# Kernel tuning notes

Hardware: AMD Instinct MI355X
Metric: run time of the kernel (lower is better)

## Reference

```python
import jax, jax.numpy as jnp
import numpy as np

EPS = 1e-12  # torch F.normalize eps

def _l2norm(x, axis):
    n = jnp.linalg.norm(x, axis=axis, keepdims=True)
    return x / jnp.maximum(n, EPS)

def setup_inputs() -> dict:
    key = jax.random.key(0)
    ks = jax.random.split(key, 4)
    B, T, C, E, I = 2, 2048, 1024, 8, 2048
    return {
        "hidden_states": jax.random.normal(ks[0], (B, T, C), dtype=jnp.float32),
        "sim_matrix": jax.random.normal(ks[1], (C, E), dtype=jnp.float32),
        "gates": jnp.zeros((E,), dtype=jnp.float32),
        "temperature": jnp.float32(1.0),
        "experts_mask": jnp.ones((E,), dtype=jnp.float32),
        "w1": jax.random.normal(ks[2], (E, C, I), dtype=jnp.float32) * (1.0 / np.sqrt(C)),
        "w2": jax.random.normal(ks[3], (E, I, C), dtype=jnp.float32) * (1.0 / np.sqrt(I)),
        "min_experts": 2,
    }

def _gating(flat_h, sim_matrix, gates, temperature, experts_mask, min_experts):
    # flat_h: [N, C]
    logit_scale = jax.nn.sigmoid(temperature)
    logits = _l2norm(flat_h, -1) @ _l2norm(sim_matrix, 0)  # [N, E]
    logits = logits * experts_mask
    gated = jax.nn.relu(logits - gates * logit_scale)
    # GateSTE: forward hard threshold, backward identity
    act = gated + jax.lax.stop_gradient((gated > 0).astype(gated.dtype) - gated)
    # fallback: tokens with no active expert get top-min_experts by logits
    inactive = jnp.sum(act, axis=1) == 0  # [N]
    _, idx = jax.lax.top_k(logits, min_experts)  # [N, k]
    fallback = jnp.sum(jax.nn.one_hot(idx, logits.shape[1], dtype=act.dtype), axis=1) > 0  # [N, E] bool
    act = jnp.where(inactive[:, None] & fallback, jnp.asarray(1.0, act.dtype), act)
    return act, logits

def reference(hidden_states, sim_matrix, gates, temperature, experts_mask, w1, w2, min_experts):
    b, t, c = hidden_states.shape
    e = w1.shape[0]
    act, router_logits = _gating(hidden_states.reshape(b * t, c), sim_matrix, gates,
                                 temperature, experts_mask, min_experts)
    inter = jnp.einsum('btc,eci->btei', hidden_states, w1)
    inter = jax.nn.gelu(inter, approximate=False)
    expert_out = jnp.einsum('btei,eic->btec', inter, w2)
    mask = act.reshape(b, t, e)
    summed = jnp.sum(expert_out * mask[..., None], axis=-2)  # [b,t,c]
    num_act = jnp.clip(jnp.sum(mask, axis=-1, keepdims=True), 1, None)
    final = summed / num_act
    return final, router_logits, act
```

## Files before the change

kernel.cpp:

```cpp
#include <hip/hip_runtime.h>
#include <math.h>

typedef __bf16 bf16x8 __attribute__((ext_vector_type(8)));
typedef __bf16 bf16x4 __attribute__((ext_vector_type(4)));
typedef float  f32x4  __attribute__((ext_vector_type(4)));

#define NTOK 4096
#define CDIM 1024
#define EEXP 8
#define IDIM 2048

__device__ __forceinline__ void async_copy16(const __bf16* g, __bf16* l) {
  __builtin_amdgcn_global_load_lds((const __attribute__((address_space(1))) void*)g,
                                   (__attribute__((address_space(3))) void*)l,
                                   16, 0, 0);
}

__device__ __forceinline__ float gelu_f(float x) {
  float u = 0.7978845608028654f * fmaf(0.044715f * x * x, x, x);
  float ex = __expf(-2.f * fabsf(u));
  float th = copysignf((1.f - ex) / (1.f + ex), u);
  return 0.5f * x * (1.f + th);
}

__global__ __launch_bounds__(256) void gating_kernel(
    const float* __restrict__ h, const float* __restrict__ sim,
    const float* __restrict__ gates, const float* __restrict__ temp,
    const float* __restrict__ emask, const int* __restrict__ minexp,
    float* __restrict__ out_logits, float* __restrict__ out_act,
    float* __restrict__ inv_num, __bf16* __restrict__ hb)
{
  const int t = blockIdx.x, tid = threadIdx.x;
  float4 hv4 = ((const float4*)(h + (size_t)t * CDIM))[tid];
  float hv[4] = {hv4.x, hv4.y, hv4.z, hv4.w};
  bf16x4 hb4 = {(__bf16)hv[0], (__bf16)hv[1], (__bf16)hv[2], (__bf16)hv[3]};
  ((bf16x4*)(hb + (size_t)t * CDIM))[tid] = hb4;

  float d[EEXP], nn[EEXP];
  #pragma unroll
  for (int e = 0; e < EEXP; ++e) { d[e] = 0.f; nn[e] = 0.f; }
  float ss = 0.f;
  #pragma unroll
  for (int j = 0; j < 4; ++j) {
    ss = fmaf(hv[j], hv[j], ss);
    const float* sr = sim + (size_t)(tid * 4 + j) * EEXP;
    float4 s0 = ((const float4*)sr)[0];
    float4 s1 = ((const float4*)sr)[1];
    float sv[8] = {s0.x, s0.y, s0.z, s0.w, s1.x, s1.y, s1.z, s1.w};
    #pragma unroll
    for (int e = 0; e < EEXP; ++e) {
      d[e]  = fmaf(hv[j], sv[e], d[e]);
      nn[e] = fmaf(sv[e], sv[e], nn[e]);
    }
  }
  #pragma unroll
  for (int off = 32; off > 0; off >>= 1) {
    ss += __shfl_down(ss, off);
    #pragma unroll
    for (int e = 0; e < EEXP; ++e) {
      d[e]  += __shfl_down(d[e], off);
      nn[e] += __shfl_down(nn[e], off);
    }
  }
  __shared__ float red[4][20];
  const int wv = tid >> 6;
  if ((tid & 63) == 0) {
    red[wv][0] = ss;
    #pragma unroll
    for (int e = 0; e < EEXP; ++e) { red[wv][1 + e] = d[e]; red[wv][9 + e] = nn[e]; }
  }
  __syncthreads();
  if (tid == 0) {
    float sst = red[0][0] + red[1][0] + red[2][0] + red[3][0];
    float inv_h = 1.f / fmaxf(sqrtf(sst), 1e-12f);
    float ls = 1.f / (1.f + expf(-temp[0]));
    float logit[EEXP], act[EEXP];
    float cnt = 0.f;
    #pragma unroll
    for (int e = 0; e < EEXP; ++e) {
      float dot = red[0][1 + e] + red[1][1 + e] + red[2][1 + e] + red[3][1 + e];
      float nne = red[0][9 + e] + red[1][9 + e] + red[2][9 + e] + red[3][9 + e];
      float inv_s = 1.f / fmaxf(sqrtf(nne), 1e-12f);
      logit[e] = dot * inv_h * inv_s * emask[e];
      float g = logit[e] - gates[e] * ls;
      act[e] = (g > 0.f) ? 1.f : 0.f;
      cnt += act[e];
    }
    if (cnt == 0.f) {
      int k = minexp[0];
      if (k > EEXP) k = EEXP;
      bool used[EEXP];
      #pragma unroll
      for (int e = 0; e < EEXP; ++e) used[e] = false;
      for (int j = 0; j < k; ++j) {
        int best = -1; float bv = 0.f;
        for (int e = 0; e < EEXP; ++e)
          if (!used[e] && (best < 0 || logit[e] > bv)) { best = e; bv = logit[e]; }
        if (best >= 0) { used[best] = true; act[best] = 1.f; cnt += 1.f; }
      }
    }
    float num = fmaxf(cnt, 1.f);
    inv_num[t] = 1.f / num;
    #pragma unroll
    for (int e = 0; e < EEXP; ++e) {
      out_logits[(size_t)t * EEXP + e] = logit[e];
      out_act[(size_t)t * EEXP + e]   = act[e];
    }
  }
}

__global__ __launch_bounds__(64) void pack_kernel(
    const float* __restrict__ out_act, int* __restrict__ counts,
    unsigned short* __restrict__ perm)
{
  const int e = blockIdx.x;
  const int lane = threadIdx.x;
  const unsigned long long ltmask = (lane == 63) ? ~0ULL >> 1 : (1ULL << lane) - 1ULL;
  int base = 0;
  for (int i = 0; i < NTOK / 64; ++i) {
    int tok = i * 64 + lane;
    bool f = out_act[(size_t)tok * EEXP + e] > 0.f;
    unsigned long long m = __ballot(f);
    if (f) perm[e * NTOK + base + __popcll(m & ltmask)] = (unsigned short)tok;
    base += __popcll(m);
  }
  if (lane == 0) counts[e] = base;
}

__global__ __launch_bounds__(256) void transpose_f32_bf16(
    const float* __restrict__ in0, __bf16* __restrict__ out0, int R, int Cc,
    long sIn, long sOut)
{
  const float* in = in0 + (size_t)blockIdx.z * sIn;
  __bf16* out = out0 + (size_t)blockIdx.z * sOut;
  __shared__ __align__(16) __bf16 tile[64][72];
  const int tid = threadIdx.x;
  const int c0 = blockIdx.x * 64, r0 = blockIdx.y * 64;
  #pragma unroll
  for (int p = 0; p < 2; ++p) {
    int lin = p * 256 + tid;
    int r = lin >> 3, c8 = (lin & 7) * 8;
    const float* src = in + (size_t)(r0 + r) * Cc + c0 + c8;
    float4 v0 = ((const float4*)src)[0];
    float4 v1 = ((const float4*)src)[1];
    bf16x8 v = {(__bf16)v0.x, (__bf16)v0.y, (__bf16)v0.z, (__bf16)v0.w,
                (__bf16)v1.x, (__bf16)v1.y, (__bf16)v1.z, (__bf16)v1.w};
    *(bf16x8*)&tile[r][c8] = v;
  }
  __syncthreads();
  #pragma unroll
  for (int p = 0; p < 2; ++p) {
    int lin = p * 256 + tid;
    int oc = lin >> 3, j8 = (lin & 7) * 8;
    bf16x8 o;
    #pragma unroll
    for (int jj = 0; jj < 8; ++jj) o[jj] = tile[j8 + jj][oc];
    *(bf16x8*)(out + (size_t)(c0 + oc) * R + r0 + j8) = o;
  }
}

template <int MODE, int NN, int KK>
__global__ __launch_bounds__(256, 4) void gemm_pk(
    const __bf16* __restrict__ A0, const __bf16* __restrict__ B0,
    const int* __restrict__ counts, const unsigned short* __restrict__ perm,
    const float* __restrict__ inv_num, void* __restrict__ Cout)
{
  const int lin = blockIdx.x;
  const int e = lin & 7;
  const int q = lin >> 3;
  const int m0 = (q & 31) * 128;
  const int n0 = (q >> 5) * 128;
  const int Me = counts[e];
  if (m0 >= Me) return;
  const int tid = threadIdx.x;
  const int wave = tid >> 6, lane = tid & 63;
  const int wm = (wave >> 1) * 64, wn = (wave & 1) * 64;
  const int quad = lane >> 4, lrow = lane & 15;
  const int srow = lane >> 2;
  const int skol = (((lane & 3) ^ ((lane >> 3) & 3)) * 8);
  const int xk = (quad ^ ((lrow >> 1) & 3)) * 8;

  __shared__ __align__(16) __bf16 As[128 * 32];
  __shared__ __align__(16) __bf16 Bs[128 * 32];
  __bf16* lA = As + wave * 1024;
  __bf16* lB = Bs + wave * 1024;

  const unsigned short* pe = perm + e * NTOK;
  const int ra0 = m0 + wave * 32 + srow;
  const int ca0 = min(ra0, Me - 1), ca1 = min(ra0 + 16, Me - 1);
  const __bf16* Ab0;
  const __bf16* Ab1;
  if (MODE == 0) {
    Ab0 = A0 + (size_t)pe[ca0] * KK + skol;
    Ab1 = A0 + (size_t)pe[ca1] * KK + skol;
  } else {
    const __bf16* Abase = A0 + (size_t)e * NTOK * KK;
    Ab0 = Abase + (size_t)ca0 * KK + skol;
    Ab1 = Abase + (size_t)ca1 * KK + skol;
  }
  const __bf16* Bb = B0 + (size_t)e * (CDIM * IDIM)
                   + (size_t)(n0 + wave * 32 + srow) * KK + skol;

  f32x4 acc[4][4] = {};

  for (int k0 = 0; k0 < KK; k0 += 32) {
    async_copy16(Ab0 + k0, lA);
    async_copy16(Ab1 + k0, lA + 512);
    async_copy16(Bb + k0, lB);
    async_copy16(Bb + (size_t)16 * KK + k0, lB + 512);
    __syncthreads();
    bf16x8 af[4], bfr[4];
    #pragma unroll
    for (int mi = 0; mi < 4; ++mi)
      af[mi] = *(const bf16x8*)(As + (wm + mi * 16 + lrow) * 32 + xk);
    #pragma unroll
    for (int ni = 0; ni < 4; ++ni)
      bfr[ni] = *(const bf16x8*)(Bs + (wn + ni * 16 + lrow) * 32 + xk);
    #pragma unroll
    for (int mi = 0; mi < 4; ++mi)
      #pragma unroll
      for (int ni = 0; ni < 4; ++ni)
        acc[mi][ni] = __builtin_amdgcn_mfma_f32_16x16x32_bf16(af[mi], bfr[ni], acc[mi][ni], 0, 0, 0);
    __syncthreads();
  }

  if (MODE == 0) {
    __bf16* O = (__bf16*)Cout + (size_t)e * NTOK * NN;
    #pragma unroll
    for (int mi = 0; mi < 4; ++mi) {
      #pragma unroll
      for (int r = 0; r < 4; ++r) {
        const int row = m0 + wm + mi * 16 + quad * 4 + r;
        const float sv = inv_num[pe[min(row, Me - 1)]];
        #pragma unroll
        for (int ni = 0; ni < 4; ++ni) {
          const int col = n0 + wn + ni * 16 + lrow;
          O[(size_t)row * NN + col] = (__bf16)(gelu_f(acc[mi][ni][r]) * sv);
        }
      }
    }
  } else {
    float* O = (float*)Cout;
    #pragma unroll
    for (int mi = 0; mi < 4; ++mi) {
      #pragma unroll
      for (int r = 0; r < 4; ++r) {
        const int row = m0 + wm + mi * 16 + quad * 4 + r;
        if (row < Me) {
          const int tok = pe[row];
          #pragma unroll
          for (int ni = 0; ni < 4; ++ni) {
            const int col = n0 + wn + ni * 16 + lrow;
            atomicAdd(&O[(size_t)tok * NN + col], acc[mi][ni][r]);
          }
        }
      }
    }
  }
}

extern "C" void kernel_launch(void* const* d_in, const int* in_sizes, int n_in,
                              void* d_out, int out_size, void* d_ws, size_t ws_size,
                              hipStream_t stream) {
  (void)in_sizes; (void)n_in; (void)out_size; (void)ws_size;
  const float* h     = (const float*)d_in[0];
  const float* sim   = (const float*)d_in[1];
  const float* gates = (const float*)d_in[2];
  const float* temp  = (const float*)d_in[3];
  const float* emask = (const float*)d_in[4];
  const float* w1    = (const float*)d_in[5];
  const float* w2    = (const float*)d_in[6];
  const int*   minexp = (const int*)d_in[7];

  float* out_final  = (float*)d_out;
  float* out_logits = out_final + (size_t)NTOK * CDIM;
  float* out_act    = out_logits + (size_t)NTOK * EEXP;

  char* ws = (char*)d_ws;
  float*          inv_num  = (float*)(ws + 0);
  int*            counts   = (int*)(ws + 16384);
  unsigned short* perm     = (unsigned short*)(ws + 16448);
  __bf16*         hb       = (__bf16*)(ws + 81984);
  __bf16*         w1T_all  = (__bf16*)(ws + 8470592);
  __bf16*         w2T_all  = (__bf16*)(ws + 42025024);
  __bf16*         inter_pk = (__bf16*)(ws + 75579456);

  const long sW = (long)CDIM * IDIM;

  hipMemsetAsync(out_final, 0, (size_t)NTOK * CDIM * sizeof(float), stream);
  transpose_f32_bf16<<<dim3(IDIM / 64, CDIM / 64, EEXP), 256, 0, stream>>>(
      w1, w1T_all, CDIM, IDIM, sW, sW);
  transpose_f32_bf16<<<dim3(CDIM / 64, IDIM / 64, EEXP), 256, 0, stream>>>(
      w2, w2T_all, IDIM, CDIM, sW, sW);
  gating_kernel<<<NTOK, 256, 0, stream>>>(h, sim, gates, temp, emask, minexp,
                                          out_logits, out_act, inv_num, hb);
  pack_kernel<<<EEXP, 64, 0, stream>>>(out_act, counts, perm);
  gemm_pk<0, IDIM, CDIM><<<EEXP * (IDIM / 128) * (NTOK / 128), 256, 0, stream>>>(
      hb, w1T_all, counts, perm, inv_num, (void*)inter_pk);
  gemm_pk<1, CDIM, IDIM><<<EEXP * (CDIM / 128) * (NTOK / 128), 256, 0, stream>>>(
      inter_pk, w2T_all, counts, perm, inv_num, (void*)out_final);
}
```

Before: 477.2 us.

## Double-buffer LDS tiles to prefetch next K-slice during MFMA compute

```diff
diff --git a/kernel.cpp b/kernel.cpp
--- a/kernel.cpp
+++ b/kernel.cpp
@@ -180,10 +180,8 @@
   const int skol = (((lane & 3) ^ ((lane >> 3) & 3)) * 8);
   const int xk = (quad ^ ((lrow >> 1) & 3)) * 8;
 
-  __shared__ __align__(16) __bf16 As[128 * 32];
-  __shared__ __align__(16) __bf16 Bs[128 * 32];
-  __bf16* lA = As + wave * 1024;
-  __bf16* lB = Bs + wave * 1024;
+  __shared__ __align__(16) __bf16 As[2][128 * 32];
+  __shared__ __align__(16) __bf16 Bs[2][128 * 32];
 
   const unsigned short* pe = perm + e * NTOK;
   const int ra0 = m0 + wave * 32 + srow;
@@ -203,25 +201,37 @@
 
   f32x4 acc[4][4] = {};
 
-  for (int k0 = 0; k0 < KK; k0 += 32) {
-    async_copy16(Ab0 + k0, lA);
-    async_copy16(Ab1 + k0, lA + 512);
-    async_copy16(Bb + k0, lB);
-    async_copy16(Bb + (size_t)16 * KK + k0, lB + 512);
+  const int woff = wave * 1024;
+  async_copy16(Ab0, &As[0][woff]);
+  async_copy16(Ab1, &As[0][woff + 512]);
+  async_copy16(Bb, &Bs[0][woff]);
+  async_copy16(Bb + (size_t)16 * KK, &Bs[0][woff + 512]);
+
+  const int stages = KK / 32;
+  for (int s = 0; s < stages; ++s) {
     __syncthreads();
+    if (s + 1 < stages) {
+      const int k1 = (s + 1) * 32;
+      const int b1 = (s + 1) & 1;
+      async_copy16(Ab0 + k1, &As[b1][woff]);
+      async_copy16(Ab1 + k1, &As[b1][woff + 512]);
+      async_copy16(Bb + k1, &Bs[b1][woff]);
+      async_copy16(Bb + (size_t)16 * KK + k1, &Bs[b1][woff + 512]);
+    }
+    const __bf16* Asb = As[s & 1];
+    const __bf16* Bsb = Bs[s & 1];
     bf16x8 af[4], bfr[4];
     #pragma unroll
     for (int mi = 0; mi < 4; ++mi)
-      af[mi] = *(const bf16x8*)(As + (wm + mi * 16 + lrow) * 32 + xk);
+      af[mi] = *(const bf16x8*)(Asb + (wm + mi * 16 + lrow) * 32 + xk);
     #pragma unroll
     for (int ni = 0; ni < 4; ++ni)
-      bfr[ni] = *(const bf16x8*)(Bs + (wn + ni * 16 + lrow) * 32 + xk);
+      bfr[ni] = *(const bf16x8*)(Bsb + (wn + ni * 16 + lrow) * 32 + xk);
     #pragma unroll
     for (int mi = 0; mi < 4; ++mi)
       #pragma unroll
       for (int ni = 0; ni < 4; ++ni)
         acc[mi][ni] = __builtin_amdgcn_mfma_f32_16x16x32_bf16(af[mi], bfr[ni], acc[mi][ni], 0, 0, 0);
-    __syncthreads();
   }
 
   if (MODE == 0) {
```

Measured after the change: 484.4 us. About the same (+1.5%).

## Load GEMM fragments directly from global memory, bypassing LDS staging

Applied to the files above, without the earlier changes.

```diff
diff --git a/kernel.cpp b/kernel.cpp
--- a/kernel.cpp
+++ b/kernel.cpp
@@ -9,12 +9,6 @@
 #define CDIM 1024
 #define EEXP 8
 #define IDIM 2048
-
-__device__ __forceinline__ void async_copy16(const __bf16* g, __bf16* l) {
-  __builtin_amdgcn_global_load_lds((const __attribute__((address_space(1))) void*)g,
-                                   (__attribute__((address_space(3))) void*)l,
-                                   16, 0, 0);
-}
 
 __device__ __forceinline__ float gelu_f(float x) {
   float u = 0.7978845608028654f * fmaf(0.044715f * x * x, x, x);
@@ -127,19 +121,30 @@
   if (lane == 0) counts[e] = base;
 }
 
-__global__ __launch_bounds__(256) void transpose_f32_bf16(
-    const float* __restrict__ in0, __bf16* __restrict__ out0, int R, int Cc,
-    long sIn, long sOut)
-{
-  const float* in = in0 + (size_t)blockIdx.z * sIn;
-  __bf16* out = out0 + (size_t)blockIdx.z * sOut;
+__global__ __launch_bounds__(256) void transpose_all(
+    const float* __restrict__ w1, const float* __restrict__ w2,
+    __bf16* __restrict__ w1T, __bf16* __restrict__ w2T)
+{
+  const int lin = blockIdx.x;
+  const int slot = lin >> 9;
+  const int t = lin & 511;
+  const float* in; __bf16* out; int Cc, c0, r0;
+  if (slot < 8) {
+    in = w1 + (size_t)slot * CDIM * IDIM;
+    out = w1T + (size_t)slot * CDIM * IDIM;
+    Cc = IDIM; c0 = (t & 31) * 64; r0 = (t >> 5) * 64;
+  } else {
+    in = w2 + (size_t)(slot - 8) * CDIM * IDIM;
+    out = w2T + (size_t)(slot - 8) * CDIM * IDIM;
+    Cc = CDIM; c0 = (t & 15) * 64; r0 = (t >> 4) * 64;
+  }
+  const int R = (slot < 8) ? CDIM : IDIM;
   __shared__ __align__(16) __bf16 tile[64][72];
   const int tid = threadIdx.x;
-  const int c0 = blockIdx.x * 64, r0 = blockIdx.y * 64;
   #pragma unroll
   for (int p = 0; p < 2; ++p) {
-    int lin = p * 256 + tid;
-    int r = lin >> 3, c8 = (lin & 7) * 8;
+    int l2 = p * 256 + tid;
+    int r = l2 >> 3, c8 = (l2 & 7) * 8;
     const float* src = in + (size_t)(r0 + r) * Cc + c0 + c8;
     float4 v0 = ((const float4*)src)[0];
     float4 v1 = ((const float4*)src)[1];
@@ -150,8 +155,8 @@
   __syncthreads();
   #pragma unroll
   for (int p = 0; p < 2; ++p) {
-    int lin = p * 256 + tid;
-    int oc = lin >> 3, j8 = (lin & 7) * 8;
+    int l2 = p * 256 + tid;
+    int oc = l2 >> 3, j8 = (l2 & 7) * 8;
     bf16x8 o;
     #pragma unroll
     for (int jj = 0; jj < 8; ++jj) o[jj] = tile[j8 + jj][oc];
@@ -160,7 +165,7 @@
 }
 
 template <int MODE, int NN, int KK>
-__global__ __launch_bounds__(256, 4) void gemm_pk(
+__global__ __launch_bounds__(256) void gemm_rd(
     const __bf16* __restrict__ A0, const __bf16* __restrict__ B0,
     const int* __restrict__ counts, const unsigned short* __restrict__ perm,
     const float* __restrict__ inv_num, void* __restrict__ Cout)
@@ -176,52 +181,37 @@
   const int wave = tid >> 6, lane = tid & 63;
   const int wm = (wave >> 1) * 64, wn = (wave & 1) * 64;
   const int quad = lane >> 4, lrow = lane & 15;
-  const int srow = lane >> 2;
-  const int skol = (((lane & 3) ^ ((lane >> 3) & 3)) * 8);
-  const int xk = (quad ^ ((lrow >> 1) & 3)) * 8;
-
-  __shared__ __align__(16) __bf16 As[128 * 32];
-  __shared__ __align__(16) __bf16 Bs[128 * 32];
-  __bf16* lA = As + wave * 1024;
-  __bf16* lB = Bs + wave * 1024;
 
   const unsigned short* pe = perm + e * NTOK;
-  const int ra0 = m0 + wave * 32 + srow;
-  const int ca0 = min(ra0, Me - 1), ca1 = min(ra0 + 16, Me - 1);
-  const __bf16* Ab0;
-  const __bf16* Ab1;
-  if (MODE == 0) {
-    Ab0 = A0 + (size_t)pe[ca0] * KK + skol;
-    Ab1 = A0 + (size_t)pe[ca1] * KK + skol;
-  } else {
-    const __bf16* Abase = A0 + (size_t)e * NTOK * KK;
-    Ab0 = Abase + (size_t)ca0 * KK + skol;
-    Ab1 = Abase + (size_t)ca1 * KK + skol;
-  }
-  const __bf16* Bb = B0 + (size_t)e * (CDIM * IDIM)
-                   + (size_t)(n0 + wave * 32 + srow) * KK + skol;
+
+  const __bf16* Arow[4];
+  #pragma unroll
+  for (int mi = 0; mi < 4; ++mi) {
+    const int row = min(m0 + wm + mi * 16 + lrow, Me - 1);
+    if (MODE == 0) Arow[mi] = A0 + (size_t)pe[row] * KK + quad * 8;
+    else           Arow[mi] = A0 + (size_t)e * NTOK * KK + (size_t)row * KK + quad * 8;
+  }
+  const __bf16* Brow[4];
+  #pragma unroll
+  for (int ni = 0; ni < 4; ++ni) {
+    const int col = n0 + wn + ni * 16 + lrow;
+    Brow[ni] = B0 + (size_t)e * (CDIM * IDIM) + (size_t)col * KK + quad * 8;
+  }
 
   f32x4 acc[4][4] = {};
 
+  #pragma unroll 2
   for (int k0 = 0; k0 < KK; k0 += 32) {
-    async_copy16(Ab0 + k0, lA);
-    async_copy16(Ab1 + k0, lA + 512);
-    async_copy16(Bb + k0, lB);
-    async_copy16(Bb + (size_t)16 * KK + k0, lB + 512);
-    __syncthreads();
     bf16x8 af[4], bfr[4];
     #pragma unroll
-    for (int mi = 0; mi < 4; ++mi)
-      af[mi] = *(const bf16x8*)(As + (wm + mi * 16 + lrow) * 32 + xk);
-    #pragma unroll
-    for (int ni = 0; ni < 4; ++ni)
-      bfr[ni] = *(const bf16x8*)(Bs + (wn + ni * 16 + lrow) * 32 + xk);
+    for (int mi = 0; mi < 4; ++mi) af[mi] = *(const bf16x8*)(Arow[mi] + k0);
+    #pragma unroll
+    for (int ni = 0; ni < 4; ++ni) bfr[ni] = *(const bf16x8*)(Brow[ni] + k0);
     #pragma unroll
     for (int mi = 0; mi < 4; ++mi)
       #pragma unroll
       for (int ni = 0; ni < 4; ++ni)
         acc[mi][ni] = __builtin_amdgcn_mfma_f32_16x16x32_bf16(af[mi], bfr[ni], acc[mi][ni], 0, 0, 0);
-    __syncthreads();
   }
 
   if (MODE == 0) {
@@ -285,18 +275,13 @@
   __bf16*         w2T_all  = (__bf16*)(ws + 42025024);
   __bf16*         inter_pk = (__bf16*)(ws + 75579456);
 
-  const long sW = (long)CDIM * IDIM;
-
   hipMemsetAsync(out_final, 0, (size_t)NTOK * CDIM * sizeof(float), stream);
-  transpose_f32_bf16<<<dim3(IDIM / 64, CDIM / 64, EEXP), 256, 0, stream>>>(
-      w1, w1T_all, CDIM, IDIM, sW, sW);
-  transpose_f32_bf16<<<dim3(CDIM / 64, IDIM / 64, EEXP), 256, 0, stream>>>(
-      w2, w2T_all, IDIM, CDIM, sW, sW);
+  transpose_all<<<16 * 512, 256, 0, stream>>>(w1, w2, w1T_all, w2T_all);
   gating_kernel<<<NTOK, 256, 0, stream>>>(h, sim, gates, temp, emask, minexp,
                                           out_logits, out_act, inv_num, hb);
   pack_kernel<<<EEXP, 64, 0, stream>>>(out_act, counts, perm);
-  gemm_pk<0, IDIM, CDIM><<<EEXP * (IDIM / 128) * (NTOK / 128), 256, 0, stream>>>(
+  gemm_rd<0, IDIM, CDIM><<<EEXP * (IDIM / 128) * (NTOK / 128), 256, 0, stream>>>(
       hb, w1T_all, counts, perm, inv_num, (void*)inter_pk);
-  gemm_pk<1, CDIM, IDIM><<<EEXP * (CDIM / 128) * (NTOK / 128), 256, 0, stream>>>(
+  gemm_rd<1, CDIM, IDIM><<<EEXP * (CDIM / 128) * (NTOK / 128), 256, 0, stream>>>(
       inter_pk, w2T_all, counts, perm, inv_num, (void*)out_final);
 }
```

Measured after the change: 880.8 us. +84.6%, slower.
